# Kernel optimization log

Hardware: AMD Instinct MI355X
Metric: run time of the kernel (lower is better)

The kernel has to match this reference:

```python
import jax, jax.numpy as jnp
import numpy as np

N = 10000
DIM = 64
F_CONST = 1.0
B_CONST = 0.1
R_CONST = 0.01


def setup_inputs() -> dict:
    key = jax.random.key(0)
    k1, k2 = jax.random.split(key)
    t = jnp.zeros((1,), dtype=jnp.float32)  # autonomous system; t unused
    x = jax.random.uniform(k1, (N, DIM), dtype=jnp.float32)
    A = jax.random.uniform(k2, (N, N), dtype=jnp.float32)
    return {"t": t, "x": x, "A": A}


def reference(t, x, A):
    # dx/dt = f - b*x - diag(A @ (r * x x^T)).reshape(-1, 1)
    # diag(A @ x x^T)_i = sum_j A_ij <x_j, x_i> = <x_i, (A @ x)_i>
    # so the interaction term is r * rowsum(x * (A @ x)) -- same math, no NxN intermediate.
    Ax = A @ x                                        # [N, DIM]
    outer = R_CONST * jnp.sum(x * Ax, axis=1, keepdims=True)  # [N, 1]
    return F_CONST - B_CONST * x - outer              # [N, DIM] via broadcast
```

## Files before the change

### kernel.cpp

```cpp
#include <hip/hip_runtime.h>
#include <stdint.h>


#define N_ROWS 10000
#define DIM 64
#define KTILE 32
#define NKT 313
#define F_CONST 1.0f
#define B_CONST 0.1f
#define R_CONST 0.01f

#define SACC_OFF_BYTES 1310720

typedef __attribute__((ext_vector_type(8))) short s16x8;
typedef __attribute__((ext_vector_type(4))) float f32x4;
typedef __attribute__((ext_vector_type(4))) uint32_t u32x4;

__device__ __forceinline__ uint32_t pack_bf16(float a, float b) {
    uint32_t ua = __builtin_bit_cast(uint32_t, a);
    uint32_t ub = __builtin_bit_cast(uint32_t, b);
    ua += 0x7FFFu + ((ua >> 16) & 1u);
    ub += 0x7FFFu + ((ub >> 16) & 1u);
    return (ua >> 16) | (ub & 0xFFFF0000u);
}

__global__ __launch_bounds__(256) void pack_x_kernel(const float* __restrict__ x,
                                                     uint32_t* __restrict__ ws,
                                                     float* __restrict__ sacc) {
    int id = blockIdx.x * 256 + threadIdx.x;
    if (id < N_ROWS) sacc[id] = 0.0f;
    int frag = id >> 6;
    int L = id & 63;
    int t = frag >> 2;
    int c = frag & 3;
    int k0 = t * KTILE + (L >> 4) * 8;
    int col = c * 16 + (L & 15);
    float v[8];
#pragma unroll
    for (int j = 0; j < 8; ++j) {
        int k = k0 + j;
        v[j] = (k < N_ROWS) ? x[k * DIM + col] : 0.0f;
    }
    u32x4 p;
    p.x = pack_bf16(v[0], v[1]);
    p.y = pack_bf16(v[2], v[3]);
    p.z = pack_bf16(v[4], v[5]);
    p.w = pack_bf16(v[6], v[7]);
    ((u32x4*)ws)[id] = p;
}

__global__ __launch_bounds__(256, 4) void gemm_dot_kernel(
    const float* __restrict__ A, const float* __restrict__ x,
    const uint32_t* __restrict__ ws, float* __restrict__ sacc) {
    int tid = threadIdx.x;
    int w = tid >> 6;
    int L = tid & 63;
    int quad = L >> 4;
    int m = L & 15;
    int rbase = blockIdx.x * 16;
    int q = blockIdx.y;
    int t0 = q * 79;
    int t1 = (q == 3) ? NKT : (t0 + 79);
    const float* Arow = A + (size_t)(rbase + m) * N_ROWS;

    f32x4 acc[4] = {{0.f, 0.f, 0.f, 0.f},
                    {0.f, 0.f, 0.f, 0.f},
                    {0.f, 0.f, 0.f, 0.f},
                    {0.f, 0.f, 0.f, 0.f}};

    for (int t = t0 + w; t < t1; t += 4) {
        int kg = t * KTILE + quad * 8;
        int ks = (kg < N_ROWS) ? kg : 0;
        f32x4 a0 = __builtin_nontemporal_load((const f32x4*)(Arow + ks));
        f32x4 a1 = __builtin_nontemporal_load(((const f32x4*)(Arow + ks)) + 1);
        const u32x4* pb = (const u32x4*)ws + (size_t)(t * 4) * 64 + L;
        u32x4 pa;
        pa.x = pack_bf16(a0.x, a0.y);
        pa.y = pack_bf16(a0.z, a0.w);
        pa.z = pack_bf16(a1.x, a1.y);
        pa.w = pack_bf16(a1.z, a1.w);
        s16x8 afrag = __builtin_bit_cast(s16x8, pa);
#pragma unroll
        for (int c = 0; c < 4; ++c) {
            s16x8 bfrag = __builtin_bit_cast(s16x8, pb[c * 64]);
            acc[c] = __builtin_amdgcn_mfma_f32_16x16x32_bf16(afrag, bfrag, acc[c], 0, 0, 0);
        }
    }

    float p[4];
#pragma unroll
    for (int r = 0; r < 4; ++r) {
        int grow = rbase + quad * 4 + r;
        const float* xr = x + (size_t)grow * DIM + m;
        p[r] = acc[0][r] * xr[0] + acc[1][r] * xr[16] +
               acc[2][r] * xr[32] + acc[3][r] * xr[48];
        p[r] += __shfl_xor(p[r], 1);
        p[r] += __shfl_xor(p[r], 2);
        p[r] += __shfl_xor(p[r], 4);
        p[r] += __shfl_xor(p[r], 8);
    }
    if (m == 0) {
#pragma unroll
        for (int r = 0; r < 4; ++r)
            atomicAdd(&sacc[rbase + quad * 4 + r], p[r]);
    }
}

__global__ __launch_bounds__(256) void finalize_kernel(const float* __restrict__ x,
                                                       const float* __restrict__ sacc,
                                                       float* __restrict__ out) {
    int id = blockIdx.x * 256 + threadIdx.x;
    f32x4 xv = ((const f32x4*)x)[id];
    float s = R_CONST * sacc[id >> 4];
    f32x4 o;
    o.x = F_CONST - B_CONST * xv.x - s;
    o.y = F_CONST - B_CONST * xv.y - s;
    o.z = F_CONST - B_CONST * xv.z - s;
    o.w = F_CONST - B_CONST * xv.w - s;
    ((f32x4*)out)[id] = o;
}

extern "C" void kernel_launch(void* const* d_in, const int* in_sizes, int n_in,
                              void* d_out, int out_size, void* d_ws, size_t ws_size,
                              hipStream_t stream) {
    const float* x = (const float*)d_in[1];
    const float* A = (const float*)d_in[2];
    float* out = (float*)d_out;
    uint32_t* ws = (uint32_t*)d_ws;
    float* sacc = (float*)((char*)d_ws + SACC_OFF_BYTES);

    pack_x_kernel<<<313, 256, 0, stream>>>(x, ws, sacc);
    gemm_dot_kernel<<<dim3(625, 4), 256, 0, stream>>>(A, x, ws, sacc);
    finalize_kernel<<<625, 256, 0, stream>>>(x, sacc, out);
}
```

Baseline: 586.6 us.

## Stage A tiles through swizzled double-buffered LDS with coalesced row loads

The GEMM kernel now loads A in 256-wide K chunks, one row per wave, with contiguous 16-byte loads per lane. It converts the values to bf16 and stores them in a XOR-swizzled, double-buffered LDS tile that MFMA fragments read from. Before this, each lane fetched 32 scattered bytes straight from a separate row. The next chunk's global loads are issued before the current chunk's MFMAs, so memory traffic overlaps with compute. K is padded to 10240, and the grid's K split drops from 4 to 2. This adds LDS traffic and a barrier per chunk.

```diff
diff --git a/kernel.cpp b/kernel.cpp
--- a/kernel.cpp
+++ b/kernel.cpp
@@ -5,7 +5,9 @@
 #define N_ROWS 10000
 #define DIM 64
 #define KTILE 32
-#define NKT 313
+#define NKT 320
+#define CHUNK_K 256
+#define CHUNKS_PER_Y 20
 #define F_CONST 1.0f
 #define B_CONST 0.1f
 #define R_CONST 0.01f
@@ -15,6 +17,7 @@
 typedef __attribute__((ext_vector_type(8))) short s16x8;
 typedef __attribute__((ext_vector_type(4))) float f32x4;
 typedef __attribute__((ext_vector_type(4))) uint32_t u32x4;
+typedef __attribute__((ext_vector_type(2))) uint32_t u32x2;
 
 __device__ __forceinline__ uint32_t pack_bf16(float a, float b) {
     uint32_t ua = __builtin_bit_cast(uint32_t, a);
@@ -52,57 +55,103 @@
 __global__ __launch_bounds__(256, 4) void gemm_dot_kernel(
     const float* __restrict__ A, const float* __restrict__ x,
     const uint32_t* __restrict__ ws, float* __restrict__ sacc) {
+    __shared__ __align__(16) unsigned short lds[2][16 * CHUNK_K];
+
     int tid = threadIdx.x;
     int w = tid >> 6;
     int L = tid & 63;
     int quad = L >> 4;
     int m = L & 15;
     int rbase = blockIdx.x * 16;
-    int q = blockIdx.y;
-    int t0 = q * 79;
-    int t1 = (q == 3) ? NKT : (t0 + 79);
-    const float* Arow = A + (size_t)(rbase + m) * N_ROWS;
+    int c0 = blockIdx.y * CHUNKS_PER_Y;
+    int c1 = c0 + CHUNKS_PER_Y;
+    const float* Ab = A + (size_t)rbase * N_ROWS;
 
     f32x4 acc[4] = {{0.f, 0.f, 0.f, 0.f},
                     {0.f, 0.f, 0.f, 0.f},
                     {0.f, 0.f, 0.f, 0.f},
                     {0.f, 0.f, 0.f, 0.f}};
 
-    for (int t = t0 + w; t < t1; t += 4) {
-        int kg = t * KTILE + quad * 8;
-        int ks = (kg < N_ROWS) ? kg : 0;
-        f32x4 a0 = __builtin_nontemporal_load((const f32x4*)(Arow + ks));
-        f32x4 a1 = __builtin_nontemporal_load(((const f32x4*)(Arow + ks)) + 1);
-        const u32x4* pb = (const u32x4*)ws + (size_t)(t * 4) * 64 + L;
-        u32x4 pa;
-        pa.x = pack_bf16(a0.x, a0.y);
-        pa.y = pack_bf16(a0.z, a0.w);
-        pa.z = pack_bf16(a1.x, a1.y);
-        pa.w = pack_bf16(a1.z, a1.w);
-        s16x8 afrag = __builtin_bit_cast(s16x8, pa);
+    {
+        f32x4 ld[4];
 #pragma unroll
-        for (int c = 0; c < 4; ++c) {
-            s16x8 bfrag = __builtin_bit_cast(s16x8, pb[c * 64]);
-            acc[c] = __builtin_amdgcn_mfma_f32_16x16x32_bf16(afrag, bfrag, acc[c], 0, 0, 0);
+        for (int i = 0; i < 4; ++i) {
+            int row = i * 4 + w;
+            int kg = c0 * CHUNK_K + L * 4;
+            int ks = (kg <= N_ROWS - 4) ? kg : (N_ROWS - 4);
+            ld[i] = __builtin_nontemporal_load((const f32x4*)(Ab + (size_t)row * N_ROWS + ks));
+        }
+#pragma unroll
+        for (int i = 0; i < 4; ++i) {
+            int row = i * 4 + w;
+            int unit = (L >> 1) ^ (row & 7);
+            u32x2 pk;
+            pk.x = pack_bf16(ld[i].x, ld[i].y);
+            pk.y = pack_bf16(ld[i].z, ld[i].w);
+            *(u32x2*)((char*)lds[0] + row * 512 + (unit << 4) + ((L & 1) << 3)) = pk;
         }
     }
+    __syncthreads();
 
-    float p[4];
+    int p = 0;
+    for (int c = c0; c < c1; ++c) {
+        f32x4 ld[4];
+        bool more = (c + 1 < c1);
+        if (more) {
+#pragma unroll
+            for (int i = 0; i < 4; ++i) {
+                int row = i * 4 + w;
+                int kg = (c + 1) * CHUNK_K + L * 4;
+                int ks = (kg <= N_ROWS - 4) ? kg : (N_ROWS - 4);
+                ld[i] = __builtin_nontemporal_load((const f32x4*)(Ab + (size_t)row * N_ROWS + ks));
+            }
+        }
+
+#pragma unroll
+        for (int u = 0; u < 2; ++u) {
+            int tt = w + 4 * u;
+            int T = c * 8 + tt;
+            int unit = (tt * 4 + quad) ^ (m & 7);
+            s16x8 afrag = *(const s16x8*)((const char*)lds[p] + m * 512 + (unit << 4));
+            const u32x4* pb = (const u32x4*)ws + (size_t)T * 256 + L;
+#pragma unroll
+            for (int cc = 0; cc < 4; ++cc) {
+                s16x8 bfrag = __builtin_bit_cast(s16x8, pb[cc * 64]);
+                acc[cc] = __builtin_amdgcn_mfma_f32_16x16x32_bf16(afrag, bfrag, acc[cc], 0, 0, 0);
+            }
+        }
+
+        if (more) {
+#pragma unroll
+            for (int i = 0; i < 4; ++i) {
+                int row = i * 4 + w;
+                int unit = (L >> 1) ^ (row & 7);
+                u32x2 pk;
+                pk.x = pack_bf16(ld[i].x, ld[i].y);
+                pk.y = pack_bf16(ld[i].z, ld[i].w);
+                *(u32x2*)((char*)lds[p ^ 1] + row * 512 + (unit << 4) + ((L & 1) << 3)) = pk;
+            }
+        }
+        __syncthreads();
+        p ^= 1;
+    }
+
+    float pr[4];
 #pragma unroll
     for (int r = 0; r < 4; ++r) {
         int grow = rbase + quad * 4 + r;
         const float* xr = x + (size_t)grow * DIM + m;
-        p[r] = acc[0][r] * xr[0] + acc[1][r] * xr[16] +
-               acc[2][r] * xr[32] + acc[3][r] * xr[48];
-        p[r] += __shfl_xor(p[r], 1);
-        p[r] += __shfl_xor(p[r], 2);
-        p[r] += __shfl_xor(p[r], 4);
-        p[r] += __shfl_xor(p[r], 8);
+        pr[r] = acc[0][r] * xr[0] + acc[1][r] * xr[16] +
+                acc[2][r] * xr[32] + acc[3][r] * xr[48];
+        pr[r] += __shfl_xor(pr[r], 1);
+        pr[r] += __shfl_xor(pr[r], 2);
+        pr[r] += __shfl_xor(pr[r], 4);
+        pr[r] += __shfl_xor(pr[r], 8);
     }
     if (m == 0) {
 #pragma unroll
         for (int r = 0; r < 4; ++r)
-            atomicAdd(&sacc[rbase + quad * 4 + r], p[r]);
+            atomicAdd(&sacc[rbase + quad * 4 + r], pr[r]);
     }
 }
 
@@ -129,7 +178,7 @@
     uint32_t* ws = (uint32_t*)d_ws;
     float* sacc = (float*)((char*)d_ws + SACC_OFF_BYTES);
 
-    pack_x_kernel<<<313, 256, 0, stream>>>(x, ws, sacc);
-    gemm_dot_kernel<<<dim3(625, 4), 256, 0, stream>>>(A, x, ws, sacc);
+    pack_x_kernel<<<320, 256, 0, stream>>>(x, ws, sacc);
+    gemm_dot_kernel<<<dim3(625, 2), 256, 0, stream>>>(A, x, ws, sacc);
     finalize_kernel<<<625, 256, 0, stream>>>(x, sacc, out);
 }
```

After: 525.7 us. 1.12x faster.
